# Performance work log

Measured on AMD Instinct MI355X. Metric: run time of the kernel, lower is better.

## Reference

```python
import math
import jax, jax.numpy as jnp
import numpy as np

N, T, D, H = 256, 128, 1024, 1024


def setup_inputs() -> dict:
    key = jax.random.key(0)
    k1, k2, k3, k4, k5 = jax.random.split(key, 5)
    x = jax.random.normal(k1, (N, T, D), dtype=jnp.float32)
    A = jax.random.normal(k2, (N, H, 4, 4), dtype=jnp.float32)
    Wx = jax.random.normal(k3, (D, 4 * H), dtype=jnp.float32) / math.sqrt(D)
    Wh = jax.random.normal(k4, (H, 4 * H), dtype=jnp.float32) / math.sqrt(H)
    Wattn = jax.random.normal(k5, (H, 4 * H), dtype=jnp.float32) / math.sqrt(H)
    b = jnp.zeros((4 * H,), dtype=jnp.float32)
    return {"x": x, "A": A, "Wx": Wx, "Wh": Wh, "Wattn": Wattn, "b": b}


def reference(x, A, Wx, Wh, Wattn, b):
    n, h = A.shape[0], A.shape[1]
    Af = A.reshape(n, h, 16)           # (N, H, 16) flattened 4x4 feature map
    h0 = Af.mean(axis=2)               # mean-pooled global feature inits h0, c0
    scale = 1.0 / math.sqrt(h)

    def step(carry, x_t):
        prev_h, prev_c = carry
        # scaled dot-product attention over 16 spatial locations
        logits = jnp.einsum("nh,nhl->nl", prev_h, Af) * scale   # (N, 16)
        w = jax.nn.softmax(logits, axis=1)
        attn = jnp.einsum("nhl,nl->nh", Af, w)                  # (N, H)
        # LSTM gates
        pre = x_t @ Wx + prev_h @ Wh + attn @ Wattn + b          # (N, 4H)
        i, f, o, g = jnp.split(pre, 4, axis=1)
        next_c = jax.nn.sigmoid(f) * prev_c + jax.nn.sigmoid(i) * jnp.tanh(g)
        next_h = jax.nn.sigmoid(o) * jnp.tanh(next_c)
        return (next_h, next_c), next_h

    xs = jnp.swapaxes(x, 0, 1)         # (T, N, D)
    _, hs = jax.lax.scan(step, (h0, h0), xs)
    return jnp.swapaxes(hs, 0, 1)      # (N, T, H)
```

## Files before the change

kernel.cpp:

```cpp
#include <hip/hip_runtime.h>
#include <hip/hip_bf16.h>

#define NB 256
#define TT 128
#define DD 1024
#define HH 1024
#define FH 4096
#define KTOT 3072

typedef __attribute__((ext_vector_type(4))) float f32x4;
typedef __attribute__((ext_vector_type(8))) short short8;
typedef __attribute__((ext_vector_type(4))) unsigned u32x4;

__device__ __forceinline__ unsigned short f2bf(float f) {
    union { float f; unsigned u; } v; v.f = f;
    unsigned u = v.u;
    u += 0x7FFFu + ((u >> 16) & 1u);
    return (unsigned short)(u >> 16);
}
__device__ __forceinline__ float bf2f(unsigned short u) {
    union { unsigned u; float f; } v; v.u = ((unsigned)u) << 16; return v.f;
}
__device__ __forceinline__ float sigm(float v) { return 1.f / (1.f + __expf(-v)); }
__device__ __forceinline__ float tanhf_(float v) { return 1.f - 2.f / (__expf(2.f * v) + 1.f); }

__device__ __forceinline__ void bmap(int bid, int& m0, int& j0) {
    int xx = bid & 7, yy = (bid >> 3) & 7, mt = bid >> 6;
    m0 = mt * 64;
    j0 = (xx * 8 + yy) * 16;
}

__device__ __forceinline__ short8 pack8(float4 v0, float4 v1) {
    short8 r;
    r[0] = (short)f2bf(v0.x); r[1] = (short)f2bf(v0.y);
    r[2] = (short)f2bf(v0.z); r[3] = (short)f2bf(v0.w);
    r[4] = (short)f2bf(v1.x); r[5] = (short)f2bf(v1.y);
    r[6] = (short)f2bf(v1.z); r[7] = (short)f2bf(v1.w);
    return r;
}

__global__ __launch_bounds__(256) void wt_prep(const float* __restrict__ Wx,
                                               const float* __restrict__ Wh,
                                               const float* __restrict__ Wattn,
                                               unsigned short* __restrict__ Wt) {
    __shared__ unsigned short tile[64][65];
    int k0 = blockIdx.x * 64;
    int c0 = blockIdx.y * 64;
    const float* src; int kl0;
    if (k0 < 1024)      { src = Wx;    kl0 = k0; }
    else if (k0 < 2048) { src = Wh;    kl0 = k0 - 1024; }
    else                { src = Wattn; kl0 = k0 - 2048; }
    int tid = threadIdx.x;
    int r = tid >> 2;
    int ch = (tid & 3) << 4;
    const float* p = src + (size_t)(kl0 + r) * FH + c0 + ch;
#pragma unroll
    for (int i = 0; i < 16; i += 4) {
        float4 v = *reinterpret_cast<const float4*>(p + i);
        tile[r][ch + i + 0] = f2bf(v.x);
        tile[r][ch + i + 1] = f2bf(v.y);
        tile[r][ch + i + 2] = f2bf(v.z);
        tile[r][ch + i + 3] = f2bf(v.w);
    }
    __syncthreads();
    alignas(16) unsigned short vals[16];
#pragma unroll
    for (int i = 0; i < 16; ++i) vals[i] = tile[ch + i][r];
    unsigned short* q = Wt + (size_t)(c0 + r) * KTOT + k0 + ch;
    *reinterpret_cast<uint4*>(q)     = *reinterpret_cast<uint4*>(&vals[0]);
    *reinterpret_cast<uint4*>(q + 8) = *reinterpret_cast<uint4*>(&vals[8]);
}

__global__ __launch_bounds__(256) void zero_buf(float* __restrict__ p, int n) {
    int i = blockIdx.x * 256 + threadIdx.x;
    if (i < n) p[i] = 0.f;
}

__global__ __launch_bounds__(256) void xconv(const float* __restrict__ x,
                                             unsigned short* __restrict__ xbf) {
    size_t i = ((size_t)blockIdx.x * 256 + threadIdx.x) * 8;
    float4 v0 = *reinterpret_cast<const float4*>(x + i);
    float4 v1 = *reinterpret_cast<const float4*>(x + i + 4);
    short8 p = pack8(v0, v1);
    *reinterpret_cast<short8*>(xbf + i) = p;
}

__global__ __launch_bounds__(256) void afT_prep(const float* __restrict__ A,
                                                unsigned short* __restrict__ AfT) {
    int n = blockIdx.x;
#pragma unroll
    for (int pass = 0; pass < 4; ++pass) {
        int hh = pass * 256 + threadIdx.x;
        const float4* p = reinterpret_cast<const float4*>(A + ((size_t)n * HH + hh) * 16);
        float4 a0 = p[0], a1 = p[1], a2 = p[2], a3 = p[3];
        float av[16] = {a0.x,a0.y,a0.z,a0.w, a1.x,a1.y,a1.z,a1.w,
                        a2.x,a2.y,a2.z,a2.w, a3.x,a3.y,a3.z,a3.w};
#pragma unroll
        for (int l = 0; l < 16; ++l)
            AfT[((size_t)n * 16 + l) * HH + hh] = f2bf(av[l]);
    }
}

__global__ __launch_bounds__(256) void g_gemm(const unsigned short* __restrict__ AfT,
                                              const unsigned short* __restrict__ Wt,
                                              unsigned short* __restrict__ G) {
    int mt = blockIdx.y;
    int ct = blockIdx.x;
    int tid = threadIdx.x;
    int w = tid >> 6, lane = tid & 63;
    int wm = w >> 1, wn = w & 1;
    int cw = lane & 15, k8 = (lane >> 4) << 3;

    const unsigned short* ap[4];
    const unsigned short* bp[4];
#pragma unroll
    for (int mf = 0; mf < 4; ++mf)
        ap[mf] = AfT + (size_t)(mt * 128 + wm * 64 + mf * 16 + cw) * HH + k8;
#pragma unroll
    for (int fn = 0; fn < 4; ++fn)
        bp[fn] = Wt + (size_t)(ct * 128 + wn * 64 + fn * 16 + cw) * KTOT + 2048 + k8;

    f32x4 acc[4][4];
#pragma unroll
    for (int mf = 0; mf < 4; ++mf)
#pragma unroll
        for (int fn = 0; fn < 4; ++fn)
#pragma unroll
            for (int e = 0; e < 4; ++e) acc[mf][fn][e] = 0.f;

#pragma unroll 4
    for (int ch = 0; ch < 32; ++ch) {
        short8 a[4], b[4];
#pragma unroll
        for (int i = 0; i < 4; ++i)
            a[i] = *reinterpret_cast<const short8*>(ap[i] + ch * 32);
#pragma unroll
        for (int i = 0; i < 4; ++i)
            b[i] = *reinterpret_cast<const short8*>(bp[i] + ch * 32);
#pragma unroll
        for (int mf = 0; mf < 4; ++mf)
#pragma unroll
            for (int fn = 0; fn < 4; ++fn)
                acc[mf][fn] = __builtin_amdgcn_mfma_f32_16x16x32_bf16(
                    a[mf], b[fn], acc[mf][fn], 0, 0, 0);
    }

    int l0 = (lane >> 4) << 2;
#pragma unroll
    for (int mf = 0; mf < 4; ++mf) {
        int n = mt * 8 + wm * 4 + mf;
#pragma unroll
        for (int fn = 0; fn < 4; ++fn) {
            int cc = ct * 128 + wn * 64 + fn * 16 + cw;
            unsigned lo = (unsigned)f2bf(acc[mf][fn][0]) | ((unsigned)f2bf(acc[mf][fn][1]) << 16);
            unsigned hi = (unsigned)f2bf(acc[mf][fn][2]) | ((unsigned)f2bf(acc[mf][fn][3]) << 16);
            uint2 val; val.x = lo; val.y = hi;
            *reinterpret_cast<uint2*>(G + ((size_t)n * FH + cc) * 16 + l0) = val;
        }
    }
}

__global__ __launch_bounds__(512) void init_kernel(const float* __restrict__ A,
                                                   float* __restrict__ c,
                                                   unsigned short* __restrict__ h0,
                                                   float* __restrict__ lg0) {
    int m0, j0; bmap(blockIdx.x, m0, j0);
    int tid = threadIdx.x;
    int r = tid >> 3, j2 = (tid & 7) * 2;
    int n = m0 + r;
    float lg[16];
#pragma unroll
    for (int l = 0; l < 16; ++l) lg[l] = 0.f;
#pragma unroll
    for (int e = 0; e < 2; ++e) {
        int j = j0 + j2 + e;
        const float4* p = reinterpret_cast<const float4*>(A + ((size_t)n * HH + j) * 16);
        float4 a0 = p[0], a1 = p[1], a2 = p[2], a3 = p[3];
        float av[16] = {a0.x,a0.y,a0.z,a0.w, a1.x,a1.y,a1.z,a1.w,
                        a2.x,a2.y,a2.z,a2.w, a3.x,a3.y,a3.z,a3.w};
        float s = 0.f;
#pragma unroll
        for (int l = 0; l < 16; ++l) s += av[l];
        float m = s * 0.0625f;
        c[(size_t)n * HH + j] = m;
        h0[(size_t)n * HH + j] = f2bf(m);
#pragma unroll
        for (int l = 0; l < 16; ++l) lg[l] += m * av[l];
    }
#pragma unroll
    for (int l = 0; l < 16; ++l) {
        lg[l] += __shfl_xor(lg[l], 1);
        lg[l] += __shfl_xor(lg[l], 2);
        lg[l] += __shfl_xor(lg[l], 4);
    }
    int l0 = (tid & 7) * 2;
    atomicAdd(&lg0[(size_t)n * 16 + l0],     lg[l0]);
    atomicAdd(&lg0[(size_t)n * 16 + l0 + 1], lg[l0 + 1]);
}

template<bool XBF>
__global__ __launch_bounds__(256, 4)
void gemm_step(const float* __restrict__ x, const unsigned short* __restrict__ xbf,
               const unsigned short* __restrict__ hprev, unsigned short* __restrict__ hnext,
               const unsigned short* __restrict__ Wt, const unsigned short* __restrict__ G,
               const unsigned short* __restrict__ AfT, const float* __restrict__ bb,
               const float* __restrict__ lgcur, float* __restrict__ lgnext,
               float* __restrict__ lgz, float* __restrict__ c,
               float* __restrict__ out, int t) {
    __shared__ float red[2][64][36];
    __shared__ float hn_s[32][16];

    const int bid = blockIdx.x;
    const int jt = (bid & 7) * 8 + ((bid >> 3) & 7);
    const int mt = bid >> 6;
    const int m0 = mt * 32, j0 = jt * 16;
    const int tid = threadIdx.x;
    const int wk = tid >> 6, lane = tid & 63;
    const int cw = lane & 15, k8 = (lane >> 4) << 3;

    const unsigned short* bp[4];
#pragma unroll
    for (int fn = 0; fn < 4; ++fn)
        bp[fn] = Wt + (size_t)(fn * 1024 + j0 + cw) * KTOT + wk * 512 + k8;

    f32x4 acc[2][4];
#pragma unroll
    for (int mf = 0; mf < 2; ++mf)
#pragma unroll
        for (int fn = 0; fn < 4; ++fn)
#pragma unroll
            for (int e = 0; e < 4; ++e) acc[mf][fn][e] = 0.f;

    if (wk < 2) {
        if (XBF) {
            const unsigned short* ap[2];
#pragma unroll
            for (int mf = 0; mf < 2; ++mf)
                ap[mf] = xbf + ((size_t)(m0 + mf * 16 + cw) * TT + t) * DD + wk * 512 + k8;
#pragma unroll 4
            for (int ch = 0; ch < 16; ++ch) {
                short8 a[2], b[4];
#pragma unroll
                for (int i = 0; i < 2; ++i)
                    a[i] = *reinterpret_cast<const short8*>(ap[i] + ch * 32);
#pragma unroll
                for (int i = 0; i < 4; ++i)
                    b[i] = *reinterpret_cast<const short8*>(bp[i] + ch * 32);
#pragma unroll
                for (int mf = 0; mf < 2; ++mf)
#pragma unroll
                    for (int fn = 0; fn < 4; ++fn)
                        acc[mf][fn] = __builtin_amdgcn_mfma_f32_16x16x32_bf16(
                            a[mf], b[fn], acc[mf][fn], 0, 0, 0);
            }
        } else {
            const float* ap[2];
#pragma unroll
            for (int mf = 0; mf < 2; ++mf)
                ap[mf] = x + ((size_t)(m0 + mf * 16 + cw) * TT + t) * DD + wk * 512 + k8;
#pragma unroll 2
            for (int ch = 0; ch < 16; ++ch) {
                short8 a[2], b[4];
#pragma unroll
                for (int i = 0; i < 2; ++i) {
                    float4 u0 = *reinterpret_cast<const float4*>(ap[i] + ch * 32);
                    float4 u1 = *reinterpret_cast<const float4*>(ap[i] + ch * 32 + 4);
                    a[i] = pack8(u0, u1);
                }
#pragma unroll
                for (int i = 0; i < 4; ++i)
                    b[i] = *reinterpret_cast<const short8*>(bp[i] + ch * 32);
#pragma unroll
                for (int mf = 0; mf < 2; ++mf)
#pragma unroll
                    for (int fn = 0; fn < 4; ++fn)
                        acc[mf][fn] = __builtin_amdgcn_mfma_f32_16x16x32_bf16(
                            a[mf], b[fn], acc[mf][fn], 0, 0, 0);
            }
        }
    } else {
        const unsigned short* ap[2];
#pragma unroll
        for (int mf = 0; mf < 2; ++mf)
            ap[mf] = hprev + (size_t)(m0 + mf * 16 + cw) * HH + (wk - 2) * 512 + k8;
#pragma unroll 4
        for (int ch = 0; ch < 16; ++ch) {
            short8 a[2], b[4];
#pragma unroll
            for (int i = 0; i < 2; ++i)
                a[i] = *reinterpret_cast<const short8*>(ap[i] + ch * 32);
#pragma unroll
            for (int i = 0; i < 4; ++i)
                b[i] = *reinterpret_cast<const short8*>(bp[i] + ch * 32);
#pragma unroll
            for (int mf = 0; mf < 2; ++mf)
#pragma unroll
                for (int fn = 0; fn < 4; ++fn)
                    acc[mf][fn] = __builtin_amdgcn_mfma_f32_16x16x32_bf16(
                        a[mf], b[fn], acc[mf][fn], 0, 0, 0);
        }
    }

    const int r0 = (lane >> 4) << 2;
    if (wk < 2) {
#pragma unroll
        for (int mf = 0; mf < 2; ++mf)
#pragma unroll
            for (int fn = 0; fn < 4; ++fn)
                *reinterpret_cast<f32x4*>(&red[wk][fn * 16 + cw][mf * 16 + r0]) = acc[mf][fn];
    }
    __syncthreads();
    if (wk >= 2) {
#pragma unroll
        for (int mf = 0; mf < 2; ++mf)
#pragma unroll
            for (int fn = 0; fn < 4; ++fn) {
                float* p = &red[wk - 2][fn * 16 + cw][mf * 16 + r0];
                f32x4 v = *reinterpret_cast<const f32x4*>(p);
                v += acc[mf][fn];
                *reinterpret_cast<f32x4*>(p) = v;
            }
    }
    __syncthreads();

    const bool zeroer = (jt == 0);
#pragma unroll
    for (int s = 0; s < 2; ++s) {
        int task = tid + s * 256;
        int er = task >> 4, ej = task & 15;
        int en = m0 + er, ejj = j0 + ej;

        const u32x4* gb = reinterpret_cast<const u32x4*>(G + ((size_t)en * FH + ejj) * 16);
        u32x4 gv[8];
#pragma unroll
        for (int g = 0; g < 4; ++g) {
            gv[g * 2]     = gb[g * 2048];
            gv[g * 2 + 1] = gb[g * 2048 + 1];
        }
        float cv = c[(size_t)en * HH + ejj];

        float sm[16];
        {
            const float4* lp = reinterpret_cast<const float4*>(lgcur + (size_t)en * 16);
            float4 s0 = lp[0], s1 = lp[1], s2 = lp[2], s3 = lp[3];
            float sv[16] = {s0.x,s0.y,s0.z,s0.w, s1.x,s1.y,s1.z,s1.w,
                            s2.x,s2.y,s2.z,s2.w, s3.x,s3.y,s3.z,s3.w};
            float mx = -1e30f;
#pragma unroll
            for (int l = 0; l < 16; ++l) { sv[l] *= 0.03125f; mx = fmaxf(mx, sv[l]); }
            float sum = 0.f;
#pragma unroll
            for (int l = 0; l < 16; ++l) { sm[l] = __expf(sv[l] - mx); sum += sm[l]; }
            float inv = 1.f / sum;
#pragma unroll
            for (int l = 0; l < 16; ++l) sm[l] *= inv;
        }

        float pre[4];
#pragma unroll
        for (int g = 0; g < 4; ++g) {
            float p = red[0][g * 16 + ej][er] + red[1][g * 16 + ej][er] + bb[g * HH + ejj];
            float d = 0.f;
#pragma unroll
            for (int q = 0; q < 4; ++q) {
                d += sm[q * 2]     * bf2f((unsigned short)(gv[g * 2][q] & 0xFFFF));
                d += sm[q * 2 + 1] * bf2f((unsigned short)(gv[g * 2][q] >> 16));
            }
#pragma unroll
            for (int q = 0; q < 4; ++q) {
                d += sm[8 + q * 2]     * bf2f((unsigned short)(gv[g * 2 + 1][q] & 0xFFFF));
                d += sm[8 + q * 2 + 1] * bf2f((unsigned short)(gv[g * 2 + 1][q] >> 16));
            }
            pre[g] = p + d;
        }

        float ig = sigm(pre[0]);
        float fg = sigm(pre[1]);
        float og = sigm(pre[2]);
        float gg = tanhf_(pre[3]);
        float cn = fg * cv + ig * gg;
        float hn = og * tanhf_(cn);
        c[(size_t)en * HH + ejj] = cn;
        hnext[(size_t)en * HH + ejj] = f2bf(hn);
        __builtin_nontemporal_store(hn, out + ((size_t)en * TT + t) * HH + ejj);
        hn_s[er][ej] = hn;
        if (zeroer) lgz[(size_t)en * 16 + ej] = 0.f;
    }
    __syncthreads();

#pragma unroll
    for (int s = 0; s < 2; ++s) {
        int task = tid + s * 256;
        int er = task >> 4, ej = task & 15;
        int en = m0 + er;
        const unsigned short* afp = AfT + ((size_t)en * 16 + ej) * HH + j0;
        uint4 q0 = *reinterpret_cast<const uint4*>(afp);
        uint4 q1 = *reinterpret_cast<const uint4*>(afp + 8);
        const unsigned* au = reinterpret_cast<const unsigned*>(&q0);
        const unsigned* av = reinterpret_cast<const unsigned*>(&q1);
        float part = 0.f;
#pragma unroll
        for (int q = 0; q < 4; ++q) {
            part += hn_s[er][q * 2]     * bf2f((unsigned short)(au[q] & 0xFFFF));
            part += hn_s[er][q * 2 + 1] * bf2f((unsigned short)(au[q] >> 16));
        }
#pragma unroll
        for (int q = 0; q < 4; ++q) {
            part += hn_s[er][8 + q * 2]     * bf2f((unsigned short)(av[q] & 0xFFFF));
            part += hn_s[er][8 + q * 2 + 1] * bf2f((unsigned short)(av[q] >> 16));
        }
        atomicAdd(&lgnext[(size_t)en * 16 + ej], part);
    }
}

extern "C" void kernel_launch(void* const* d_in, const int* in_sizes, int n_in,
                              void* d_out, int out_size, void* d_ws, size_t ws_size,
                              hipStream_t stream) {
    const float* x     = (const float*)d_in[0];
    const float* A     = (const float*)d_in[1];
    const float* Wx    = (const float*)d_in[2];
    const float* Wh    = (const float*)d_in[3];
    const float* Wattn = (const float*)d_in[4];
    const float* bptr  = (const float*)d_in[5];
    float* out = (float*)d_out;

    char* ws = (char*)d_ws;
    unsigned short* Wt   = (unsigned short*)(ws);
    unsigned short* G    = (unsigned short*)(ws + 25165824);
    unsigned short* AfT  = (unsigned short*)(ws + 58720256);
    unsigned short* hbuf = (unsigned short*)(ws + 67108864);
    float* c             = (float*)(ws + 68157440);
    float* lg            = (float*)(ws + 69206016);
    unsigned short* xbf  = (unsigned short*)(ws + 69255168);
    bool use_xbf = ws_size >= (size_t)69255168 + 67108864;

    wt_prep<<<dim3(48, 64), 256, 0, stream>>>(Wx, Wh, Wattn, Wt);
    zero_buf<<<48, 256, 0, stream>>>(lg, 3 * NB * 16);
    afT_prep<<<NB, 256, 0, stream>>>(A, AfT);
    g_gemm<<<dim3(32, 32), 256, 0, stream>>>(AfT, Wt, G);
    init_kernel<<<256, 512, 0, stream>>>(A, c, hbuf, lg);
    if (use_xbf) xconv<<<16384, 256, 0, stream>>>(x, xbf);

    for (int t = 0; t < TT; ++t) {
        const unsigned short* hp = hbuf + (size_t)(t & 1) * NB * HH;
        unsigned short* hx       = hbuf + (size_t)((t & 1) ^ 1) * NB * HH;
        const float* lgc = lg + (size_t)(t % 3) * NB * 16;
        float* lgn       = lg + (size_t)((t + 1) % 3) * NB * 16;
        float* lgzz      = lg + (size_t)((t + 2) % 3) * NB * 16;
        if (use_xbf)
            gemm_step<true><<<512, 256, 0, stream>>>(x, xbf, hp, hx, Wt, G, AfT, bptr,
                                                     lgc, lgn, lgzz, c, out, t);
        else
            gemm_step<false><<<512, 256, 0, stream>>>(x, xbf, hp, hx, Wt, G, AfT, bptr,
                                                      lgc, lgn, lgzz, c, out, t);
    }
}
```

Before: 4.264 ms.

## Precompute x@Wx for all timesteps in one large GEMM before recurrence

Adds a single batched bf16 MFMA GEMM that computes x_t@Wx plus bias for every timestep up front, storing the result in fp32 or bf16 depending on workspace size. The per-step kernel then only does the h@Wh product over K=1024 instead of K=2048 (with Wattn folded via G), using smaller 16-row tiles and 1024 blocks. This moves the input projection off the serial critical path into one highly parallel GEMM. The cost is a large workspace buffer (256–512 MB) and extra memory traffic to read it back each step, and the new path is only taken if the workspace is big enough.

```diff
diff --git a/kernel.cpp b/kernel.cpp
--- a/kernel.cpp
+++ b/kernel.cpp
@@ -160,6 +160,72 @@
     }
 }
 
+template<bool PF32>
+__global__ __launch_bounds__(256)
+void xw_gemm(const float* __restrict__ x, const unsigned short* __restrict__ Wt,
+             const float* __restrict__ bb, void* __restrict__ prex) {
+    int ct = blockIdx.x;
+    int mt = blockIdx.y;
+    int tid = threadIdx.x;
+    int w = tid >> 6, lane = tid & 63;
+    int wm = w >> 1, wn = w & 1;
+    int cw = lane & 15, k8 = (lane >> 4) << 3;
+
+    const float* ap[4];
+    const unsigned short* bp[4];
+#pragma unroll
+    for (int mf = 0; mf < 4; ++mf)
+        ap[mf] = x + (size_t)(mt * 128 + wm * 64 + mf * 16 + cw) * DD + k8;
+#pragma unroll
+    for (int fn = 0; fn < 4; ++fn)
+        bp[fn] = Wt + (size_t)(ct * 128 + wn * 64 + fn * 16 + cw) * KTOT + k8;
+
+    f32x4 acc[4][4];
+#pragma unroll
+    for (int mf = 0; mf < 4; ++mf)
+#pragma unroll
+        for (int fn = 0; fn < 4; ++fn)
+#pragma unroll
+            for (int e = 0; e < 4; ++e) acc[mf][fn][e] = 0.f;
+
+#pragma unroll 2
+    for (int ch = 0; ch < 32; ++ch) {
+        short8 a[4]; short8 b[4];
+#pragma unroll
+        for (int i = 0; i < 4; ++i) {
+            float4 u0 = *reinterpret_cast<const float4*>(ap[i] + ch * 32);
+            float4 u1 = *reinterpret_cast<const float4*>(ap[i] + ch * 32 + 4);
+            a[i] = pack8(u0, u1);
+        }
+#pragma unroll
+        for (int i = 0; i < 4; ++i)
+            b[i] = *reinterpret_cast<const short8*>(bp[i] + ch * 32);
+#pragma unroll
+        for (int mf = 0; mf < 4; ++mf)
+#pragma unroll
+            for (int fn = 0; fn < 4; ++fn)
+                acc[mf][fn] = __builtin_amdgcn_mfma_f32_16x16x32_bf16(
+                    a[mf], b[fn], acc[mf][fn], 0, 0, 0);
+    }
+
+    int r0 = (lane >> 4) << 2;
+#pragma unroll
+    for (int fn = 0; fn < 4; ++fn) {
+        int cc = ct * 128 + wn * 64 + fn * 16 + cw;
+        float bv = bb[cc];
+#pragma unroll
+        for (int mf = 0; mf < 4; ++mf) {
+            size_t row = (size_t)(mt * 128 + wm * 64 + mf * 16 + r0);
+#pragma unroll
+            for (int e = 0; e < 4; ++e) {
+                float v = acc[mf][fn][e] + bv;
+                if (PF32) ((float*)prex)[(row + e) * FH + cc] = v;
+                else      ((unsigned short*)prex)[(row + e) * FH + cc] = f2bf(v);
+            }
+        }
+    }
+}
+
 __global__ __launch_bounds__(512) void init_kernel(const float* __restrict__ A,
                                                    float* __restrict__ c,
                                                    unsigned short* __restrict__ h0,
@@ -196,6 +262,156 @@
     int l0 = (tid & 7) * 2;
     atomicAdd(&lg0[(size_t)n * 16 + l0],     lg[l0]);
     atomicAdd(&lg0[(size_t)n * 16 + l0 + 1], lg[l0 + 1]);
+}
+
+template<bool PF32>
+__global__ __launch_bounds__(256, 4)
+void step_prex(const void* __restrict__ prex,
+               const unsigned short* __restrict__ hprev, unsigned short* __restrict__ hnext,
+               const unsigned short* __restrict__ Wt, const unsigned short* __restrict__ G,
+               const unsigned short* __restrict__ AfT,
+               const float* __restrict__ lgcur, float* __restrict__ lgnext,
+               float* __restrict__ lgz, float* __restrict__ c,
+               float* __restrict__ out, int t) {
+    __shared__ float red[2][64][20];
+    __shared__ float hn_s[16][16];
+
+    const int bid = blockIdx.x;
+    const int jt = (bid & 7) * 8 + ((bid >> 3) & 7);
+    const int mt = bid >> 6;
+    const int m0 = mt * 16, j0 = jt * 16;
+    const int tid = threadIdx.x;
+    const int wk = tid >> 6, lane = tid & 63;
+    const int cw = lane & 15, k8 = (lane >> 4) << 3;
+
+    const unsigned short* bp[4];
+#pragma unroll
+    for (int fn = 0; fn < 4; ++fn)
+        bp[fn] = Wt + (size_t)(fn * 1024 + j0 + cw) * KTOT + 1024 + wk * 256 + k8;
+    const unsigned short* ap = hprev + (size_t)(m0 + cw) * HH + wk * 256 + k8;
+
+    f32x4 acc[4];
+#pragma unroll
+    for (int fn = 0; fn < 4; ++fn)
+#pragma unroll
+        for (int e = 0; e < 4; ++e) acc[fn][e] = 0.f;
+
+#pragma unroll
+    for (int ch = 0; ch < 8; ++ch) {
+        short8 a = *reinterpret_cast<const short8*>(ap + ch * 32);
+        short8 b[4];
+#pragma unroll
+        for (int i = 0; i < 4; ++i)
+            b[i] = *reinterpret_cast<const short8*>(bp[i] + ch * 32);
+#pragma unroll
+        for (int fn = 0; fn < 4; ++fn)
+            acc[fn] = __builtin_amdgcn_mfma_f32_16x16x32_bf16(a, b[fn], acc[fn], 0, 0, 0);
+    }
+
+    const int r0 = (lane >> 4) << 2;
+    if (wk < 2) {
+#pragma unroll
+        for (int fn = 0; fn < 4; ++fn)
+            *reinterpret_cast<f32x4*>(&red[wk][fn * 16 + cw][r0]) = acc[fn];
+    }
+    __syncthreads();
+    if (wk >= 2) {
+#pragma unroll
+        for (int fn = 0; fn < 4; ++fn) {
+            float* p = &red[wk - 2][fn * 16 + cw][r0];
+            f32x4 v = *reinterpret_cast<const f32x4*>(p);
+            v += acc[fn];
+            *reinterpret_cast<f32x4*>(p) = v;
+        }
+    }
+    __syncthreads();
+
+    const int er = tid >> 4, ej = tid & 15;
+    const int en = m0 + er, ejj = j0 + ej;
+
+    const u32x4* gb = reinterpret_cast<const u32x4*>(G + ((size_t)en * FH + ejj) * 16);
+    u32x4 gv[8];
+#pragma unroll
+    for (int g = 0; g < 4; ++g) {
+        gv[g * 2]     = gb[g * 2048];
+        gv[g * 2 + 1] = gb[g * 2048 + 1];
+    }
+    float pxv[4];
+    {
+        size_t prow = ((size_t)en * TT + t) * FH + ejj;
+#pragma unroll
+        for (int g = 0; g < 4; ++g) {
+            if (PF32) pxv[g] = ((const float*)prex)[prow + g * 1024];
+            else      pxv[g] = bf2f(((const unsigned short*)prex)[prow + g * 1024]);
+        }
+    }
+    float cv = c[(size_t)en * HH + ejj];
+
+    float sm[16];
+    {
+        const float4* lp = reinterpret_cast<const float4*>(lgcur + (size_t)en * 16);
+        float4 s0 = lp[0], s1 = lp[1], s2 = lp[2], s3 = lp[3];
+        float sv[16] = {s0.x,s0.y,s0.z,s0.w, s1.x,s1.y,s1.z,s1.w,
+                        s2.x,s2.y,s2.z,s2.w, s3.x,s3.y,s3.z,s3.w};
+        float mx = -1e30f;
+#pragma unroll
+        for (int l = 0; l < 16; ++l) { sv[l] *= 0.03125f; mx = fmaxf(mx, sv[l]); }
+        float sum = 0.f;
+#pragma unroll
+        for (int l = 0; l < 16; ++l) { sm[l] = __expf(sv[l] - mx); sum += sm[l]; }
+        float inv = 1.f / sum;
+#pragma unroll
+        for (int l = 0; l < 16; ++l) sm[l] *= inv;
+    }
+
+    float pre[4];
+#pragma unroll
+    for (int g = 0; g < 4; ++g) {
+        float p = red[0][g * 16 + ej][er] + red[1][g * 16 + ej][er] + pxv[g];
+        float d = 0.f;
+#pragma unroll
+        for (int q = 0; q < 4; ++q) {
+            d += sm[q * 2]     * bf2f((unsigned short)(gv[g * 2][q] & 0xFFFF));
+            d += sm[q * 2 + 1] * bf2f((unsigned short)(gv[g * 2][q] >> 16));
+        }
+#pragma unroll
+        for (int q = 0; q < 4; ++q) {
+            d += sm[8 + q * 2]     * bf2f((unsigned short)(gv[g * 2 + 1][q] & 0xFFFF));
+            d += sm[8 + q * 2 + 1] * bf2f((unsigned short)(gv[g * 2 + 1][q] >> 16));
+        }
+        pre[g] = p + d;
+    }
+
+    float ig = sigm(pre[0]);
+    float fg = sigm(pre[1]);
+    float og = sigm(pre[2]);
+    float gg = tanhf_(pre[3]);
+    float cn = fg * cv + ig * gg;
+    float hn = og * tanhf_(cn);
+    c[(size_t)en * HH + ejj] = cn;
+    hnext[(size_t)en * HH + ejj] = f2bf(hn);
+    __builtin_nontemporal_store(hn, out + ((size_t)en * TT + t) * HH + ejj);
+    hn_s[er][ej] = hn;
+    if (jt == 0) lgz[(size_t)en * 16 + ej] = 0.f;
+    __syncthreads();
+
+    const unsigned short* afp = AfT + ((size_t)en * 16 + ej) * HH + j0;
+    uint4 q0 = *reinterpret_cast<const uint4*>(afp);
+    uint4 q1 = *reinterpret_cast<const uint4*>(afp + 8);
+    const unsigned* au = reinterpret_cast<const unsigned*>(&q0);
+    const unsigned* av = reinterpret_cast<const unsigned*>(&q1);
+    float part = 0.f;
+#pragma unroll
+    for (int q = 0; q < 4; ++q) {
+        part += hn_s[er][q * 2]     * bf2f((unsigned short)(au[q] & 0xFFFF));
+        part += hn_s[er][q * 2 + 1] * bf2f((unsigned short)(au[q] >> 16));
+    }
+#pragma unroll
+    for (int q = 0; q < 4; ++q) {
+        part += hn_s[er][8 + q * 2]     * bf2f((unsigned short)(av[q] & 0xFFFF));
+        part += hn_s[er][8 + q * 2 + 1] * bf2f((unsigned short)(av[q] >> 16));
+    }
+    atomicAdd(&lgnext[(size_t)en * 16 + ej], part);
 }
 
 template<bool XBF>
@@ -431,15 +647,22 @@
     unsigned short* hbuf = (unsigned short*)(ws + 67108864);
     float* c             = (float*)(ws + 68157440);
     float* lg            = (float*)(ws + 69206016);
-    unsigned short* xbf  = (unsigned short*)(ws + 69255168);
-    bool use_xbf = ws_size >= (size_t)69255168 + 67108864;
+    const size_t base = 69255168;
+    void* prex = (void*)(ws + base);
+    unsigned short* xbf = (unsigned short*)(ws + base);
+
+    bool prex32 = ws_size >= base + (size_t)536870912;
+    bool prex16 = !prex32 && ws_size >= base + (size_t)268435456;
+    bool use_xbf = !prex32 && !prex16 && ws_size >= base + (size_t)67108864;
 
     wt_prep<<<dim3(48, 64), 256, 0, stream>>>(Wx, Wh, Wattn, Wt);
     zero_buf<<<48, 256, 0, stream>>>(lg, 3 * NB * 16);
     afT_prep<<<NB, 256, 0, stream>>>(A, AfT);
     g_gemm<<<dim3(32, 32), 256, 0, stream>>>(AfT, Wt, G);
     init_kernel<<<256, 512, 0, stream>>>(A, c, hbuf, lg);
-    if (use_xbf) xconv<<<16384, 256, 0, stream>>>(x, xbf);
+    if (prex32)      xw_gemm<true><<<dim3(32, 256), 256, 0, stream>>>(x, Wt, bptr, prex);
+    else if (prex16) xw_gemm<false><<<dim3(32, 256), 256, 0, stream>>>(x, Wt, bptr, prex);
+    else if (use_xbf) xconv<<<16384, 256, 0, stream>>>(x, xbf);
 
     for (int t = 0; t < TT; ++t) {
         const unsigned short* hp = hbuf + (size_t)(t & 1) * NB * HH;
@@ -447,7 +670,13 @@
         const float* lgc = lg + (size_t)(t % 3) * NB * 16;
         float* lgn       = lg + (size_t)((t + 1) % 3) * NB * 16;
         float* lgzz      = lg + (size_t)((t + 2) % 3) * NB * 16;
-        if (use_xbf)
+        if (prex32)
+            step_prex<true><<<1024, 256, 0, stream>>>(prex, hp, hx, Wt, G, AfT,
+                                                      lgc, lgn, lgzz, c, out, t);
+        else if (prex16)
+            step_prex<false><<<1024, 256, 0, stream>>>(prex, hp, hx, Wt, G, AfT,
+                                                       lgc, lgn, lgzz, c, out, t);
+        else if (use_xbf)
             gemm_step<true><<<512, 256, 0, stream>>>(x, xbf, hp, hx, Wt, G, AfT, bptr,
                                                      lgc, lgn, lgzz, c, out, t);
         else
```

After: 4.818 ms. +13.0%, slower.

## Halve step row tile and replace logit atomics with per-tile partial buffers

Applied to the files above, without the earlier changes.

Each step kernel now covers 16 rows instead of 32, so 1024 blocks launch instead of 512 and each thread handles one output element. The attention-logit accumulation no longer uses atomicAdd plus a rotating zeroed buffer. Each column tile writes its partial to a [n][l][64] buffer, and the next step reduces the 64 partials. This removes atomics and the zeroing launch, adds parallelism, and adds a 64-wide reduction read per block. Weight reuse per block is halved, so weight traffic through cache doubles.

```diff
diff --git a/kernel.cpp b/kernel.cpp
--- a/kernel.cpp
+++ b/kernel.cpp
@@ -7,6 +7,7 @@
 #define HH 1024
 #define FH 4096
 #define KTOT 3072
+#define LGN (NB * 16 * 64)
 
 typedef __attribute__((ext_vector_type(4))) float f32x4;
 typedef __attribute__((ext_vector_type(8))) short short8;
@@ -71,11 +72,6 @@
     *reinterpret_cast<uint4*>(q + 8) = *reinterpret_cast<uint4*>(&vals[8]);
 }
 
-__global__ __launch_bounds__(256) void zero_buf(float* __restrict__ p, int n) {
-    int i = blockIdx.x * 256 + threadIdx.x;
-    if (i < n) p[i] = 0.f;
-}
-
 __global__ __launch_bounds__(256) void xconv(const float* __restrict__ x,
                                              unsigned short* __restrict__ xbf) {
     size_t i = ((size_t)blockIdx.x * 256 + threadIdx.x) * 8;
@@ -163,8 +159,9 @@
 __global__ __launch_bounds__(512) void init_kernel(const float* __restrict__ A,
                                                    float* __restrict__ c,
                                                    unsigned short* __restrict__ h0,
-                                                   float* __restrict__ lg0) {
+                                                   float* __restrict__ lgp0) {
     int m0, j0; bmap(blockIdx.x, m0, j0);
+    int jt = j0 >> 4;
     int tid = threadIdx.x;
     int r = tid >> 3, j2 = (tid & 7) * 2;
     int n = m0 + r;
@@ -194,223 +191,191 @@
         lg[l] += __shfl_xor(lg[l], 4);
     }
     int l0 = (tid & 7) * 2;
-    atomicAdd(&lg0[(size_t)n * 16 + l0],     lg[l0]);
-    atomicAdd(&lg0[(size_t)n * 16 + l0 + 1], lg[l0 + 1]);
+    lgp0[((size_t)n * 16 + l0)     * 64 + jt] = lg[l0];
+    lgp0[((size_t)n * 16 + l0 + 1) * 64 + jt] = lg[l0 + 1];
 }
 
 template<bool XBF>
 __global__ __launch_bounds__(256, 4)
-void gemm_step(const float* __restrict__ x, const unsigned short* __restrict__ xbf,
+void lstm_step(const float* __restrict__ x, const unsigned short* __restrict__ xbf,
                const unsigned short* __restrict__ hprev, unsigned short* __restrict__ hnext,
                const unsigned short* __restrict__ Wt, const unsigned short* __restrict__ G,
                const unsigned short* __restrict__ AfT, const float* __restrict__ bb,
                const float* __restrict__ lgcur, float* __restrict__ lgnext,
-               float* __restrict__ lgz, float* __restrict__ c,
-               float* __restrict__ out, int t) {
-    __shared__ float red[2][64][36];
-    __shared__ float hn_s[32][16];
+               float* __restrict__ c, float* __restrict__ out, int t) {
+    __shared__ float red[2][64][20];
+    __shared__ float smlg[16][17];
+    __shared__ float hn_s[16][16];
 
     const int bid = blockIdx.x;
     const int jt = (bid & 7) * 8 + ((bid >> 3) & 7);
     const int mt = bid >> 6;
-    const int m0 = mt * 32, j0 = jt * 16;
+    const int m0 = mt * 16, j0 = jt * 16;
     const int tid = threadIdx.x;
     const int wk = tid >> 6, lane = tid & 63;
     const int cw = lane & 15, k8 = (lane >> 4) << 3;
 
+    {
+        int er = tid >> 4, l = tid & 15;
+        const float4* lp = reinterpret_cast<const float4*>(
+            lgcur + ((size_t)(m0 + er) * 16 + l) * 64);
+        float a0 = 0.f, a1 = 0.f, a2 = 0.f, a3 = 0.f;
+#pragma unroll
+        for (int q = 0; q < 16; ++q) {
+            float4 v = lp[q];
+            a0 += v.x; a1 += v.y; a2 += v.z; a3 += v.w;
+        }
+        smlg[er][l] = (a0 + a1) + (a2 + a3);
+    }
+
     const unsigned short* bp[4];
+    const int kb = (wk < 2) ? wk * 512 : 1024 + (wk - 2) * 512;
 #pragma unroll
     for (int fn = 0; fn < 4; ++fn)
-        bp[fn] = Wt + (size_t)(fn * 1024 + j0 + cw) * KTOT + wk * 512 + k8;
-
-    f32x4 acc[2][4];
-#pragma unroll
-    for (int mf = 0; mf < 2; ++mf)
-#pragma unroll
-        for (int fn = 0; fn < 4; ++fn)
-#pragma unroll
-            for (int e = 0; e < 4; ++e) acc[mf][fn][e] = 0.f;
+        bp[fn] = Wt + (size_t)(fn * 1024 + j0 + cw) * KTOT + kb + k8;
+
+    f32x4 acc[4];
+#pragma unroll
+    for (int fn = 0; fn < 4; ++fn)
+#pragma unroll
+        for (int e = 0; e < 4; ++e) acc[fn][e] = 0.f;
 
     if (wk < 2) {
         if (XBF) {
-            const unsigned short* ap[2];
-#pragma unroll
-            for (int mf = 0; mf < 2; ++mf)
-                ap[mf] = xbf + ((size_t)(m0 + mf * 16 + cw) * TT + t) * DD + wk * 512 + k8;
+            const unsigned short* ap = xbf + ((size_t)(m0 + cw) * TT + t) * DD + wk * 512 + k8;
 #pragma unroll 4
             for (int ch = 0; ch < 16; ++ch) {
-                short8 a[2], b[4];
-#pragma unroll
-                for (int i = 0; i < 2; ++i)
-                    a[i] = *reinterpret_cast<const short8*>(ap[i] + ch * 32);
+                short8 a = *reinterpret_cast<const short8*>(ap + ch * 32);
+                short8 b[4];
 #pragma unroll
                 for (int i = 0; i < 4; ++i)
                     b[i] = *reinterpret_cast<const short8*>(bp[i] + ch * 32);
 #pragma unroll
-                for (int mf = 0; mf < 2; ++mf)
-#pragma unroll
-                    for (int fn = 0; fn < 4; ++fn)
-                        acc[mf][fn] = __builtin_amdgcn_mfma_f32_16x16x32_bf16(
-                            a[mf], b[fn], acc[mf][fn], 0, 0, 0);
+                for (int fn = 0; fn < 4; ++fn)
+                    acc[fn] = __builtin_amdgcn_mfma_f32_16x16x32_bf16(a, b[fn], acc[fn], 0, 0, 0);
             }
         } else {
-            const float* ap[2];
-#pragma unroll
-            for (int mf = 0; mf < 2; ++mf)
-                ap[mf] = x + ((size_t)(m0 + mf * 16 + cw) * TT + t) * DD + wk * 512 + k8;
+            const float* ap = x + ((size_t)(m0 + cw) * TT + t) * DD + wk * 512 + k8;
 #pragma unroll 2
             for (int ch = 0; ch < 16; ++ch) {
-                short8 a[2], b[4];
-#pragma unroll
-                for (int i = 0; i < 2; ++i) {
-                    float4 u0 = *reinterpret_cast<const float4*>(ap[i] + ch * 32);
-                    float4 u1 = *reinterpret_cast<const float4*>(ap[i] + ch * 32 + 4);
-                    a[i] = pack8(u0, u1);
-                }
+                float4 u0 = *reinterpret_cast<const float4*>(ap + ch * 32);
+                float4 u1 = *reinterpret_cast<const float4*>(ap + ch * 32 + 4);
+                short8 a = pack8(u0, u1);
+                short8 b[4];
 #pragma unroll
                 for (int i = 0; i < 4; ++i)
                     b[i] = *reinterpret_cast<const short8*>(bp[i] + ch * 32);
 #pragma unroll
-                for (int mf = 0; mf < 2; ++mf)
-#pragma unroll
-                    for (int fn = 0; fn < 4; ++fn)
-                        acc[mf][fn] = __builtin_amdgcn_mfma_f32_16x16x32_bf16(
-                            a[mf], b[fn], acc[mf][fn], 0, 0, 0);
+                for (int fn = 0; fn < 4; ++fn)
+                    acc[fn] = __builtin_amdgcn_mfma_f32_16x16x32_bf16(a, b[fn], acc[fn], 0, 0, 0);
             }
         }
     } else {
-        const unsigned short* ap[2];
-#pragma unroll
-        for (int mf = 0; mf < 2; ++mf)
-            ap[mf] = hprev + (size_t)(m0 + mf * 16 + cw) * HH + (wk - 2) * 512 + k8;
+        const unsigned short* ap = hprev + (size_t)(m0 + cw) * HH + (wk - 2) * 512 + k8;
 #pragma unroll 4
         for (int ch = 0; ch < 16; ++ch) {
-            short8 a[2], b[4];
-#pragma unroll
-            for (int i = 0; i < 2; ++i)
-                a[i] = *reinterpret_cast<const short8*>(ap[i] + ch * 32);
+            short8 a = *reinterpret_cast<const short8*>(ap + ch * 32);
+            short8 b[4];
 #pragma unroll
             for (int i = 0; i < 4; ++i)
                 b[i] = *reinterpret_cast<const short8*>(bp[i] + ch * 32);
 #pragma unroll
-            for (int mf = 0; mf < 2; ++mf)
-#pragma unroll
-                for (int fn = 0; fn < 4; ++fn)
-                    acc[mf][fn] = __builtin_amdgcn_mfma_f32_16x16x32_bf16(
-                        a[mf], b[fn], acc[mf][fn], 0, 0, 0);
+            for (int fn = 0; fn < 4; ++fn)
+                acc[fn] = __builtin_amdgcn_mfma_f32_16x16x32_bf16(a, b[fn], acc[fn], 0, 0, 0);
         }
     }
 
     const int r0 = (lane >> 4) << 2;
     if (wk < 2) {
 #pragma unroll
-        for (int mf = 0; mf < 2; ++mf)
-#pragma unroll
-            for (int fn = 0; fn < 4; ++fn)
-                *reinterpret_cast<f32x4*>(&red[wk][fn * 16 + cw][mf * 16 + r0]) = acc[mf][fn];
+        for (int fn = 0; fn < 4; ++fn)
+            *reinterpret_cast<f32x4*>(&red[wk][fn * 16 + cw][r0]) = acc[fn];
     }
     __syncthreads();
     if (wk >= 2) {
 #pragma unroll
-        for (int mf = 0; mf < 2; ++mf)
-#pragma unroll
-            for (int fn = 0; fn < 4; ++fn) {
-                float* p = &red[wk - 2][fn * 16 + cw][mf * 16 + r0];
-                f32x4 v = *reinterpret_cast<const f32x4*>(p);
-                v += acc[mf][fn];
-                *reinterpret_cast<f32x4*>(p) = v;
-            }
+        for (int fn = 0; fn < 4; ++fn) {
+            float* p = &red[wk - 2][fn * 16 + cw][r0];
+            f32x4 v = *reinterpret_cast<const f32x4*>(p);
+            v += acc[fn];
+            *reinterpret_cast<f32x4*>(p) = v;
+        }
     }
     __syncthreads();
 
-    const bool zeroer = (jt == 0);
-#pragma unroll
-    for (int s = 0; s < 2; ++s) {
-        int task = tid + s * 256;
-        int er = task >> 4, ej = task & 15;
-        int en = m0 + er, ejj = j0 + ej;
-
-        const u32x4* gb = reinterpret_cast<const u32x4*>(G + ((size_t)en * FH + ejj) * 16);
-        u32x4 gv[8];
-#pragma unroll
-        for (int g = 0; g < 4; ++g) {
-            gv[g * 2]     = gb[g * 2048];
-            gv[g * 2 + 1] = gb[g * 2048 + 1];
-        }
-        float cv = c[(size_t)en * HH + ejj];
-
-        float sm[16];
-        {
-            const float4* lp = reinterpret_cast<const float4*>(lgcur + (size_t)en * 16);
-            float4 s0 = lp[0], s1 = lp[1], s2 = lp[2], s3 = lp[3];
-            float sv[16] = {s0.x,s0.y,s0.z,s0.w, s1.x,s1.y,s1.z,s1.w,
-                            s2.x,s2.y,s2.z,s2.w, s3.x,s3.y,s3.z,s3.w};
-            float mx = -1e30f;
-#pragma unroll
-            for (int l = 0; l < 16; ++l) { sv[l] *= 0.03125f; mx = fmaxf(mx, sv[l]); }
-            float sum = 0.f;
-#pragma unroll
-            for (int l = 0; l < 16; ++l) { sm[l] = __expf(sv[l] - mx); sum += sm[l]; }
-            float inv = 1.f / sum;
-#pragma unroll
-            for (int l = 0; l < 16; ++l) sm[l] *= inv;
-        }
-
-        float pre[4];
-#pragma unroll
-        for (int g = 0; g < 4; ++g) {
-            float p = red[0][g * 16 + ej][er] + red[1][g * 16 + ej][er] + bb[g * HH + ejj];
-            float d = 0.f;
-#pragma unroll
-            for (int q = 0; q < 4; ++q) {
-                d += sm[q * 2]     * bf2f((unsigned short)(gv[g * 2][q] & 0xFFFF));
-                d += sm[q * 2 + 1] * bf2f((unsigned short)(gv[g * 2][q] >> 16));
-            }
-#pragma unroll
-            for (int q = 0; q < 4; ++q) {
-                d += sm[8 + q * 2]     * bf2f((unsigned short)(gv[g * 2 + 1][q] & 0xFFFF));
-                d += sm[8 + q * 2 + 1] * bf2f((unsigned short)(gv[g * 2 + 1][q] >> 16));
-            }
-            pre[g] = p + d;
-        }
-
-        float ig = sigm(pre[0]);
-        float fg = sigm(pre[1]);
-        float og = sigm(pre[2]);
-        float gg = tanhf_(pre[3]);
-        float cn = fg * cv + ig * gg;
-        float hn = og * tanhf_(cn);
-        c[(size_t)en * HH + ejj] = cn;
-        hnext[(size_t)en * HH + ejj] = f2bf(hn);
-        __builtin_nontemporal_store(hn, out + ((size_t)en * TT + t) * HH + ejj);
-        hn_s[er][ej] = hn;
-        if (zeroer) lgz[(size_t)en * 16 + ej] = 0.f;
-    }
+    const int er = tid >> 4, ej = tid & 15;
+    const int en = m0 + er, ejj = j0 + ej;
+
+    const u32x4* gb = reinterpret_cast<const u32x4*>(G + ((size_t)en * FH + ejj) * 16);
+    u32x4 gv[8];
+#pragma unroll
+    for (int g = 0; g < 4; ++g) {
+        gv[g * 2]     = gb[g * 2048];
+        gv[g * 2 + 1] = gb[g * 2048 + 1];
+    }
+    float cv = c[(size_t)en * HH + ejj];
+
+    float sm[16];
+    {
+        float mx = -1e30f;
+        float sv[16];
+#pragma unroll
+        for (int l = 0; l < 16; ++l) { sv[l] = smlg[er][l] * 0.03125f; mx = fmaxf(mx, sv[l]); }
+        float sum = 0.f;
+#pragma unroll
+        for (int l = 0; l < 16; ++l) { sm[l] = __expf(sv[l] - mx); sum += sm[l]; }
+        float inv = 1.f / sum;
+#pragma unroll
+        for (int l = 0; l < 16; ++l) sm[l] *= inv;
+    }
+
+    float pre[4];
+#pragma unroll
+    for (int g = 0; g < 4; ++g) {
+        float p = red[0][g * 16 + ej][er] + red[1][g * 16 + ej][er] + bb[g * HH + ejj];
+        float d = 0.f;
+#pragma unroll
+        for (int q = 0; q < 4; ++q) {
+            d += sm[q * 2]     * bf2f((unsigned short)(gv[g * 2][q] & 0xFFFF));
+            d += sm[q * 2 + 1] * bf2f((unsigned short)(gv[g * 2][q] >> 16));
+        }
+#pragma unroll
+        for (int q = 0; q < 4; ++q) {
+            d += sm[8 + q * 2]     * bf2f((unsigned short)(gv[g * 2 + 1][q] & 0xFFFF));
+            d += sm[8 + q * 2 + 1] * bf2f((unsigned short)(gv[g * 2 + 1][q] >> 16));
+        }
+        pre[g] = p + d;
+    }
+
+    float ig = sigm(pre[0]);
+    float fg = sigm(pre[1]);
+    float og = sigm(pre[2]);
+    float gg = tanhf_(pre[3]);
+    float cn = fg * cv + ig * gg;
+    float hn = og * tanhf_(cn);
+    c[(size_t)en * HH + ejj] = cn;
+    hnext[(size_t)en * HH + ejj] = f2bf(hn);
+    __builtin_nontemporal_store(hn, out + ((size_t)en * TT + t) * HH + ejj);
+    hn_s[er][ej] = hn;
     __syncthreads();
 
-#pragma unroll
-    for (int s = 0; s < 2; ++s) {
-        int task = tid + s * 256;
-        int er = task >> 4, ej = task & 15;
-        int en = m0 + er;
-        const unsigned short* afp = AfT + ((size_t)en * 16 + ej) * HH + j0;
-        uint4 q0 = *reinterpret_cast<const uint4*>(afp);
-        uint4 q1 = *reinterpret_cast<const uint4*>(afp + 8);
-        const unsigned* au = reinterpret_cast<const unsigned*>(&q0);
-        const unsigned* av = reinterpret_cast<const unsigned*>(&q1);
-        float part = 0.f;
-#pragma unroll
-        for (int q = 0; q < 4; ++q) {
-            part += hn_s[er][q * 2]     * bf2f((unsigned short)(au[q] & 0xFFFF));
-            part += hn_s[er][q * 2 + 1] * bf2f((unsigned short)(au[q] >> 16));
-        }
-#pragma unroll
-        for (int q = 0; q < 4; ++q) {
-            part += hn_s[er][8 + q * 2]     * bf2f((unsigned short)(av[q] & 0xFFFF));
-            part += hn_s[er][8 + q * 2 + 1] * bf2f((unsigned short)(av[q] >> 16));
-        }
-        atomicAdd(&lgnext[(size_t)en * 16 + ej], part);
-    }
+    const unsigned short* afp = AfT + ((size_t)en * 16 + ej) * HH + j0;
+    uint4 q0 = *reinterpret_cast<const uint4*>(afp);
+    uint4 q1 = *reinterpret_cast<const uint4*>(afp + 8);
+    const unsigned* au = reinterpret_cast<const unsigned*>(&q0);
+    const unsigned* av = reinterpret_cast<const unsigned*>(&q1);
+    float part = 0.f;
+#pragma unroll
+    for (int q = 0; q < 4; ++q) {
+        part += hn_s[er][q * 2]     * bf2f((unsigned short)(au[q] & 0xFFFF));
+        part += hn_s[er][q * 2 + 1] * bf2f((unsigned short)(au[q] >> 16));
+    }
+#pragma unroll
+    for (int q = 0; q < 4; ++q) {
+        part += hn_s[er][8 + q * 2]     * bf2f((unsigned short)(av[q] & 0xFFFF));
+        part += hn_s[er][8 + q * 2 + 1] * bf2f((unsigned short)(av[q] >> 16));
+    }
+    lgnext[((size_t)en * 16 + ej) * 64 + jt] = part;
 }
 
 extern "C" void kernel_launch(void* const* d_in, const int* in_sizes, int n_in,
@@ -430,28 +395,26 @@
     unsigned short* AfT  = (unsigned short*)(ws + 58720256);
     unsigned short* hbuf = (unsigned short*)(ws + 67108864);
     float* c             = (float*)(ws + 68157440);
-    float* lg            = (float*)(ws + 69206016);
-    unsigned short* xbf  = (unsigned short*)(ws + 69255168);
-    bool use_xbf = ws_size >= (size_t)69255168 + 67108864;
+    float* lgp           = (float*)(ws + 69206016);
+    unsigned short* xbf  = (unsigned short*)(ws + 71303168);
+    bool use_xbf = ws_size >= (size_t)71303168 + 67108864;
 
     wt_prep<<<dim3(48, 64), 256, 0, stream>>>(Wx, Wh, Wattn, Wt);
-    zero_buf<<<48, 256, 0, stream>>>(lg, 3 * NB * 16);
     afT_prep<<<NB, 256, 0, stream>>>(A, AfT);
     g_gemm<<<dim3(32, 32), 256, 0, stream>>>(AfT, Wt, G);
-    init_kernel<<<256, 512, 0, stream>>>(A, c, hbuf, lg);
+    init_kernel<<<256, 512, 0, stream>>>(A, c, hbuf, lgp);
     if (use_xbf) xconv<<<16384, 256, 0, stream>>>(x, xbf);
 
     for (int t = 0; t < TT; ++t) {
         const unsigned short* hp = hbuf + (size_t)(t & 1) * NB * HH;
         unsigned short* hx       = hbuf + (size_t)((t & 1) ^ 1) * NB * HH;
-        const float* lgc = lg + (size_t)(t % 3) * NB * 16;
-        float* lgn       = lg + (size_t)((t + 1) % 3) * NB * 16;
-        float* lgzz      = lg + (size_t)((t + 2) % 3) * NB * 16;
+        const float* lgc = lgp + (size_t)(t & 1) * LGN;
+        float* lgn       = lgp + (size_t)((t + 1) & 1) * LGN;
         if (use_xbf)
-            gemm_step<true><<<512, 256, 0, stream>>>(x, xbf, hp, hx, Wt, G, AfT, bptr,
-                                                     lgc, lgn, lgzz, c, out, t);
+            lstm_step<true><<<1024, 256, 0, stream>>>(x, xbf, hp, hx, Wt, G, AfT, bptr,
+                                                      lgc, lgn, c, out, t);
         else
-            gemm_step<false><<<512, 256, 0, stream>>>(x, xbf, hp, hx, Wt, G, AfT, bptr,
-                                                      lgc, lgn, lgzz, c, out, t);
-    }
-}
+            lstm_step<false><<<1024, 256, 0, stream>>>(x, xbf, hp, hx, Wt, G, AfT, bptr,
+                                                       lgc, lgn, c, out, t);
+    }
+}
```

Result: slower. 6.710 ms (+57.4%).
